# Kernel tuning notes

Measured on AMD Instinct MI355X. Metric: run time of the kernel, lower is better.

## Reference

```python
import jax, jax.numpy as jnp
import numpy as np
from jax import lax

N_CLASS = 21          # VOC: 20 foreground + background
SCORE_THRESH = 0.05   # 'evaluate' preset
NMS_THRESH = 0.3


def loc2bbox(src_bbox, loc):
    # src_bbox, loc: [N, 4] in (y1, x1, y2, x2) / (dy, dx, dh, dw)
    h = src_bbox[:, 2] - src_bbox[:, 0]
    w = src_bbox[:, 3] - src_bbox[:, 1]
    cy = src_bbox[:, 0] + 0.5 * h
    cx = src_bbox[:, 1] + 0.5 * w
    dy, dx, dh, dw = loc[:, 0], loc[:, 1], loc[:, 2], loc[:, 3]
    ncy = dy * h + cy
    ncx = dx * w + cx
    nh = jnp.exp(dh) * h
    nw = jnp.exp(dw) * w
    return jnp.stack([ncy - 0.5 * nh, ncx - 0.5 * nw,
                      ncy + 0.5 * nh, ncx + 0.5 * nw], axis=1)


def pairwise_iou(boxes):
    # boxes: [R, 4] (y1, x1, y2, x2) -> [R, R]
    area = (boxes[:, 2] - boxes[:, 0]) * (boxes[:, 3] - boxes[:, 1])
    ty1 = jnp.maximum(boxes[:, None, 0], boxes[None, :, 0])
    tx1 = jnp.maximum(boxes[:, None, 1], boxes[None, :, 1])
    ty2 = jnp.minimum(boxes[:, None, 2], boxes[None, :, 2])
    tx2 = jnp.minimum(boxes[:, None, 3], boxes[None, :, 3])
    inter = jnp.clip(ty2 - ty1, 0) * jnp.clip(tx2 - tx1, 0)
    union = area[:, None] + area[None, :] - inter
    return inter / jnp.maximum(union, 1e-10)


def nms_keep(boxes, scores):
    # boxes [R,4], scores [R] for one class. Returns bool keep mask [R]
    # (score-thresholded + greedy NMS), fixed shape (mask instead of gather).
    R = boxes.shape[0]
    valid = scores > SCORE_THRESH
    order = jnp.argsort(-scores)
    b = boxes[order]
    v = valid[order]
    suppress = pairwise_iou(b) > NMS_THRESH  # [R, R]
    idx = jnp.arange(R)

    def body(i, keep):
        sup_by_earlier = jnp.any(keep & suppress[:, i] & (idx < i))
        return keep.at[i].set(v[i] & ~sup_by_earlier)

    keep_sorted = lax.fori_loop(0, R, body, jnp.zeros((R,), bool))
    return jnp.zeros((R,), bool).at[order].set(keep_sorted)


def setup_inputs() -> dict:
    key = jax.random.key(0)
    k1, k2, k3, k4 = jax.random.split(key, 4)
    R = 2000
    size_h, size_w = 600, 800
    roi_cls_loc = jax.random.normal(k1, (R, N_CLASS * 4), jnp.float32)
    roi_scores = jax.random.normal(k2, (R, N_CLASS), jnp.float32)
    # valid (y1, x1, y2, x2) rois inside the image
    yx = jax.random.uniform(k3, (R, 2), jnp.float32) * jnp.array([size_h - 32.0, size_w - 32.0])
    hw = 16.0 + jax.random.uniform(k4, (R, 2), jnp.float32) * 128.0
    rois = jnp.concatenate([yx, yx + hw], axis=1)
    return {"roi_cls_loc": roi_cls_loc, "roi_scores": roi_scores,
            "rois": rois, "size_h": size_h, "size_w": size_w}


def reference(roi_cls_loc, roi_scores, rois, size_h, size_w):
    R = rois.shape[0]
    mean = jnp.tile(jnp.asarray([0.0, 0.0, 0.0, 0.0], roi_cls_loc.dtype), N_CLASS)
    std = jnp.tile(jnp.asarray([0.1, 0.1, 0.2, 0.2], roi_cls_loc.dtype), N_CLASS)
    loc = roi_cls_loc * std + mean                      # [R, 4*C]
    loc = loc.reshape(R * N_CLASS, 4)
    src = jnp.broadcast_to(rois[:, None, :], (R, N_CLASS, 4)).reshape(R * N_CLASS, 4)
    box = loc2bbox(src, loc).reshape(R, N_CLASS, 4)
    # clamp y coords (0,2) to [0, H], x coords (1,3) to [0, W]
    y = jnp.clip(box[..., 0::2], 0.0, float(size_h))
    x = jnp.clip(box[..., 1::2], 0.0, float(size_w))
    box = jnp.stack([y[..., 0], x[..., 0], y[..., 1], x[..., 1]], axis=-1)
    prob = jax.nn.softmax(roi_scores, axis=1)           # [R, C]
    # foreground classes only (skip background class 0)
    cls_box = jnp.transpose(box[:, 1:, :], (1, 0, 2))   # [C-1, R, 4]
    cls_prob = prob[:, 1:].T                            # [C-1, R]
    keep = jax.vmap(nms_keep)(lax.stop_gradient(cls_box),
                              lax.stop_gradient(cls_prob))  # [C-1, R] bool
    kept = keep.astype(box.dtype)[..., None]
    # fixed-shape detections: per-class boxes + score, zeroed where suppressed
    out = jnp.concatenate([cls_box * kept, cls_prob[..., None] * kept], axis=-1)
    return out  # [C-1, R, 5]
```

## Files before the change

### kernel.cpp

```cpp
#include <hip/hip_runtime.h>
#include <math.h>

#define NCLS 21
#define NCO 20
#define SUB 8
#define TPB 256
#define STH 1024
#define RCAP 2048
#define RMAX 2000
#define LDSW 7680
#define SCORE_THRESH 0.05f

typedef unsigned long long u64;
typedef unsigned int u32;
typedef unsigned short u16;

#define IOU_MID (20132661.0 / 67108864.0)

__device__ __forceinline__ u64 readlane64(u64 v, int l) {
    u32 lo = (u32)__builtin_amdgcn_readlane((int)(u32)v, l);
    u32 hi = (u32)__builtin_amdgcn_readlane((int)(u32)(v >> 32), l);
    return ((u64)hi << 32) | lo;
}
__device__ __forceinline__ float readlanef(float v, int l) {
    return __uint_as_float((u32)__builtin_amdgcn_readlane((int)__float_as_uint(v), l));
}
__device__ __forceinline__ u64 shflxor64(u64 v, int m) {
    u32 lo = (u32)__shfl_xor((int)(u32)v, m, 64);
    u32 hi = (u32)__shfl_xor((int)(u32)(v >> 32), m, 64);
    return ((u64)hi << 32) | lo;
}

__device__ __forceinline__ int coff(int ic, int nw) {
    return ((ic * nw - ((ic * (ic - 1)) >> 1)) << 6);
}

__device__ __forceinline__ void decode_box(
    const float* __restrict__ rois, const float* __restrict__ loc,
    int r, int cls, float sh, float sw,
    float& by1, float& bx1, float& by2, float& bx2)
{
    float4 rb = *(const float4*)(rois + r * 4);
    float y1 = rb.x, x1 = rb.y, y2 = rb.z, x2 = rb.w;
    float h = y2 - y1, w = x2 - x1;
    float cy = y1 + 0.5f * h, cx = x1 + 0.5f * w;
    float4 l4 = *(const float4*)(loc + r * (NCLS * 4) + cls * 4);
    float dy = l4.x * 0.1f, dx = l4.y * 0.1f;
    float dh = l4.z * 0.2f, dw = l4.w * 0.2f;
    float ncy = dy * h + cy, ncx = dx * w + cx;
    float nh = expf(dh) * h, nw = expf(dw) * w;
    by1 = fminf(fmaxf(ncy - 0.5f * nh, 0.f), sh);
    bx1 = fminf(fmaxf(ncx - 0.5f * nw, 0.f), sw);
    by2 = fminf(fmaxf(ncy + 0.5f * nh, 0.f), sh);
    bx2 = fminf(fmaxf(ncx + 0.5f * nw, 0.f), sw);
}

__device__ __forceinline__ float softmax_p(
    const float* __restrict__ scores, int r, int cls)
{
    const float* srow = scores + r * NCLS;
    float s[NCLS];
    float4 a0 = *(const float4*)(srow);
    float4 a1 = *(const float4*)(srow + 4);
    float4 a2 = *(const float4*)(srow + 8);
    float4 a3 = *(const float4*)(srow + 12);
    float4 a4 = *(const float4*)(srow + 16);
    s[0]=a0.x; s[1]=a0.y; s[2]=a0.z; s[3]=a0.w;
    s[4]=a1.x; s[5]=a1.y; s[6]=a1.z; s[7]=a1.w;
    s[8]=a2.x; s[9]=a2.y; s[10]=a2.z; s[11]=a2.w;
    s[12]=a3.x; s[13]=a3.y; s[14]=a3.z; s[15]=a3.w;
    s[16]=a4.x; s[17]=a4.y; s[18]=a4.z; s[19]=a4.w;
    s[20]=srow[20];
    float m = -INFINITY;
#pragma unroll
    for (int k = 0; k < NCLS; ++k) m = fmaxf(m, s[k]);
    float sum = 0.f, ec = 0.f;
#pragma unroll
    for (int k = 0; k < NCLS; ++k) {
        float e = expf(s[k] - m);
        sum += e;
        if (k == cls) ec = e;
    }
    return ec / sum;
}

__global__ __launch_bounds__(STH) void sort_kernel(
    const float* __restrict__ scores, u64* __restrict__ ord,
    int* __restrict__ nvv, int R)
{
    __shared__ u64 vkey[RCAP];
    __shared__ int cnt;
    const int t = threadIdx.x;
    const int c = blockIdx.x;
    const int lane = t & 63;
    if (t == 0) cnt = 0;
    __syncthreads();

    for (int r = t; r < R; r += STH) {
        float p = softmax_p(scores, r, c + 1);
        bool valid = (p > SCORE_THRESH);
        u64 key = ((u64)(~__float_as_uint(p)) << 32) | (u32)r;
        u64 bal = __ballot(valid);
        if (bal) {
            int nb = (int)__popcll(bal);
            int base = 0;
            if (lane == 0) base = atomicAdd(&cnt, nb);
            base = __shfl(base, 0, 64);
            if (valid)
                vkey[base + (int)__popcll(bal & ((1ull << lane) - 1ull))] = key;
        }
    }
    __syncthreads();
    const int nv = cnt;
    if (t == 0) nvv[c] = nv;

    for (int ibase = 0; ibase < nv; ibase += STH) {
        int i = ibase + t;
        if (i < nv) {
            u64 kj = vkey[i];
            int rank = 0;
#pragma unroll 4
            for (int j = 0; j < nv; ++j)
                rank += (vkey[j] < kj);
            ord[((size_t)c << 11) + rank] = kj;
        }
    }
}

__global__ __launch_bounds__(TPB) void mask_kernel(
    const float* __restrict__ loc, const float* __restrict__ rois,
    const int* __restrict__ ph, const int* __restrict__ pw,
    const u64* __restrict__ ord, const int* __restrict__ nvv,
    u64* __restrict__ M, int R)
{
    __shared__ float4 pb[RCAP];
    __shared__ float ar[RCAP];
    const int t = threadIdx.x;
    const int c = blockIdx.x >> 3;
    const int s = blockIdx.x & 7;
    const int nv = nvv[c];
    const int nw = (nv + 63) >> 6;
    const float sh = (float)(*ph), sw = (float)(*pw);

    for (int i = t; i < nv; i += TPB) {
        u64 key = ord[((size_t)c << 11) + i];
        int r = (int)(u32)key;
        float a0, a1, a2, a3;
        decode_box(rois, loc, r, c + 1, sh, sw, a0, a1, a2, a3);
        pb[i] = make_float4(a0, a1, a2, a3);
        ar[i] = (a2 - a0) * (a3 - a1);
    }
    __syncthreads();

    const int lane = t & 63;
    const int wid = (s << 2) | (t >> 6);
    const int ntasks = nw * (nw + 1) / 2;
    u64* Mc = M + ((size_t)c << 16);
    for (int task = wid; task < ntasks; task += SUB * 4) {
        int ic = 0, rm = task;
        while (rm >= nw - ic) { rm -= nw - ic; ++ic; }
        int v = ic + rm;
        int i = (ic << 6) + lane;
        float4 a = pb[i];
        float iarea = ar[i];
        float4 rj = pb[(v << 6) + lane];
        float ja_l = ar[(v << 6) + lane];
        int jcnt = min(64, nv - (v << 6));
        u64 m = 0;
        for (int jj = 0; jj < jcnt; ++jj) {
            float jy1 = readlanef(rj.x, jj);
            float jx1 = readlanef(rj.y, jj);
            float jy2 = readlanef(rj.z, jj);
            float jx2 = readlanef(rj.w, jj);
            float ja  = readlanef(ja_l, jj);
            float ty1 = fmaxf(a.x, jy1);
            float tx1 = fmaxf(a.y, jx1);
            float ty2 = fminf(a.z, jy2);
            float tx2 = fminf(a.w, jx2);
            float inter = fmaxf(ty2 - ty1, 0.f) * fmaxf(tx2 - tx1, 0.f);
            float uni = fmaxf(iarea + ja - inter, 1e-10f);
            if ((double)inter > IOU_MID * (double)uni) m |= 1ull << jj;
        }
        if (v == ic) m &= (lane < 63) ? (~0ull << (lane + 1)) : 0ull;
        int W = nw - ic;
        if (i < nv) Mc[coff(ic, nw) + lane * W + (v - ic)] = m;
    }
}

__global__ __launch_bounds__(TPB) void resolveout_kernel(
    const float* __restrict__ loc, const float* __restrict__ rois,
    const int* __restrict__ ph, const int* __restrict__ pw,
    const u64* __restrict__ ord, const int* __restrict__ nvv,
    const u64* __restrict__ M, float* __restrict__ out, int R)
{
    __shared__ u64 mlds[LDSW];
    __shared__ u64 keptw[32];
    const int t = threadIdx.x;
    const int c = blockIdx.x >> 3;
    const int s = blockIdx.x & 7;
    const int nv = nvv[c];
    const int nw = (nv + 63) >> 6;
    const u64* Mc = M + ((size_t)c << 16);
    const int S = coff(nw, nw);
    const bool lds_ok = (S <= LDSW);
    if (t < 32) keptw[t] = 0;

    if (lds_ok) {
        for (int base = 0; base < S; base += 2048) {
            u64 v[8];
#pragma unroll
            for (int j = 0; j < 8; ++j) {
                int k = base + (j << 8) + t;
                v[j] = (k < S) ? Mc[k] : 0ull;
            }
#pragma unroll
            for (int j = 0; j < 8; ++j) {
                int k = base + (j << 8) + t;
                if (k < S) mlds[k] = v[j];
            }
        }
    }
    __syncthreads();

    if (t < 64) {
        const int lane = t;
        auto core = [&](const auto* B) {
            u64 remreg = 0;
            for (int w = 0; w < nw; ++w) {
                const int W = nw - w;
                const int cb = coff(w, nw);
                int i = (w << 6) + lane;
                u64 cw = (i < nv) ? B[cb + lane * W] : 0ull;
                int remn = nv - (w << 6);
                u64 vb = (remn >= 64) ? ~0ull : ((1ull << remn) - 1ull);
                u64 cand = vb & ~readlane64(remreg, w);
                u64 X = cand;
                if (X) {
                    for (int it = 0; it < 64; ++it) {
                        u64 contrib = ((X >> lane) & 1ull) ? cw : 0ull;
#pragma unroll
                        for (int d = 1; d < 64; d <<= 1)
                            contrib |= shflxor64(contrib, d);
                        bool keep = ((cand >> lane) & 1ull) &&
                                    !((contrib >> lane) & 1ull);
                        u64 Xn = __ballot(keep);
                        if (Xn == X) break;
                        X = Xn;
                    }
                    if (lane == 0) keptw[w] = X;
                    bool lact = (lane > w) && (lane < nw);
                    u64 km = X, acc = 0;
                    while (km) {
                        int bs[8];
#pragma unroll
                        for (int g = 0; g < 8; ++g) {
                            bs[g] = km ? (__ffsll(km) - 1) : -1;
                            if (km) km &= km - 1;
                        }
                        u64 tmp[8];
#pragma unroll
                        for (int g = 0; g < 8; ++g)
                            tmp[g] = (bs[g] >= 0 && lact)
                                ? B[cb + bs[g] * W + (lane - w)] : 0ull;
#pragma unroll
                        for (int g = 0; g < 8; ++g) acc |= tmp[g];
                    }
                    if (lact) remreg |= acc;
                }
            }
        };
        if (lds_ok) core(mlds); else core(Mc);
    }
    __syncthreads();

    const int chunk = (R + 7) >> 3;
    const int r0 = s * chunk;
    const int r1 = min(R, r0 + chunk);
    float* slice = out + (size_t)c * R * 5;
    for (int k = r0 * 5 + t; k < r1 * 5; k += TPB) slice[k] = 0.f;
    __syncthreads();

    const float sh = (float)(*ph), sw = (float)(*pw);
    for (int i = t; i < nv; i += TPB) {
        if ((keptw[i >> 6] >> (i & 63)) & 1ull) {
            u64 key = ord[((size_t)c << 11) + i];
            int r = (int)(u32)key;
            if (r >= r0 && r < r1) {
                float v0, v1, v2, v3;
                decode_box(rois, loc, r, c + 1, sh, sw, v0, v1, v2, v3);
                float* p = slice + (size_t)r * 5;
                p[0] = v0; p[1] = v1; p[2] = v2; p[3] = v3;
                p[4] = __uint_as_float(~(u32)(key >> 32));
            }
        }
    }
}

#define NTH 1024
__global__ __launch_bounds__(NTH) void fused_kernel(
    const float* __restrict__ loc, const float* __restrict__ scores,
    const float* __restrict__ rois, const int* __restrict__ ph,
    const int* __restrict__ pw, float* __restrict__ out, int R)
{
    __shared__ u64 vkey[RMAX];
    __shared__ float2 p1[RMAX], p2[RMAX];
    __shared__ u64 chunk[64 * 33];
    __shared__ u64 rem[32];
    __shared__ int cnt;

    const int t = threadIdx.x;
    const int lane = t & 63;
    const int c = blockIdx.x + 1;
    const float sh = (float)(*ph), sw = (float)(*pw);

    if (t == 0) cnt = 0;
    if (t < 32) rem[t] = 0;
    __syncthreads();

    for (int r = t; r < R; r += NTH) {
        float p = softmax_p(scores, r, c);
        if (p > SCORE_THRESH) {
            int j = atomicAdd(&cnt, 1);
            vkey[j] = ((u64)(~__float_as_uint(p)) << 32) | (u32)r;
        }
    }
    __syncthreads();
    const int nv = cnt;
    const int nw = (nv + 63) >> 6;

    u64 kk0 = 0, kk1 = 0;
    int r0 = 0, r1 = 0;
    bool in0 = (t < nv), in1 = (t + NTH < nv);
    if (in0) kk0 = vkey[t];
    if (in1) kk1 = vkey[t + NTH];
#pragma unroll 8
    for (int i = 0; i < nv; ++i) {
        u64 k = vkey[i];
        r0 += (k < kk0);
        r1 += (k < kk1);
    }
    __syncthreads();

    for (int u = 0; u < 2; ++u) {
        bool act = u ? in1 : in0;
        if (act) {
            u64 kk = u ? kk1 : kk0;
            int rank = u ? r1 : r0;
            int r = (int)(kk & 0xffffffffu);
            float b0, b1, b2, b3;
            decode_box(rois, loc, r, c, sh, sw, b0, b1, b2, b3);
            vkey[rank] = kk;
            p1[rank] = make_float2(b0, b1);
            p2[rank] = make_float2(b2, b3);
        }
    }
    __syncthreads();

    for (int w = 0; w < nw; ++w) {
        int nwr = nw - w;
        u64 remw = rem[w];
        for (int task = t; task < (nwr << 6); task += NTH) {
            int vr = task >> 6, il = task & 63;
            int i = (w << 6) + il;
            u64 m = 0;
            if (i < nv && !((remw >> il) & 1ull)) {
                int v = w + vr;
                u64 rv = rem[v];
                if (~rv != 0ull) {
                    float2 a1 = p1[i], a2 = p2[i];
                    float iarea = (a2.x - a1.x) * (a2.y - a1.y);
                    int j0 = v << 6;
                    int jhi = min(64, nv - j0);
#pragma unroll 4
                    for (int jj = 0; jj < jhi; ++jj) {
                        float2 b1 = p1[j0 + jj], b2 = p2[j0 + jj];
                        float ty1 = fmaxf(a1.x, b1.x);
                        float tx1 = fmaxf(a1.y, b1.y);
                        float ty2 = fminf(a2.x, b2.x);
                        float tx2 = fminf(a2.y, b2.y);
                        float inter = fmaxf(ty2 - ty1, 0.f) * fmaxf(tx2 - tx1, 0.f);
                        float jarea = (b2.x - b1.x) * (b2.y - b1.y);
                        float uni = fmaxf(iarea + jarea - inter, 1e-10f);
                        if ((double)inter > IOU_MID * (double)uni) m |= 1ull << jj;
                    }
                    if (vr == 0)
                        m &= (il < 63) ? (~0ull << (il + 1)) : 0ull;
                }
            }
            chunk[il * 33 + vr] = m;
        }
        __syncthreads();

        u64 cand = chunk[lane * 33];
        u64 cur = rem[w];
        int remn = nv - (w << 6);
        u64 vb = (remn >= 64) ? ~0ull : ((1ull << remn) - 1ull);
        u64 avail = vb & ~cur;
        u64 kept = 0;
        while (avail) {
            int bb = __ffsll(avail) - 1;
            kept |= 1ull << bb;
            cur |= __shfl(cand, bb, 64);
            avail &= ~(cur | (1ull << bb));
        }
        int vr = t & 31, pg = t >> 5;
        if (vr >= 1 && vr < nwr) {
            u64 acc = 0, km = kept;
            int n = 0;
            while (km) {
                int bb = __ffsll(km) - 1;
                km &= km - 1;
                if ((n & 31) == pg) acc |= chunk[bb * 33 + vr];
                ++n;
            }
            if (acc) atomicOr(&rem[w + vr], acc);
        }
        if (t == 0) rem[w] = cur;
        __syncthreads();
    }

    u16* inv = (u16*)chunk;
    for (int r = t; r < R; r += NTH) inv[r] = 0xffffu;
    __syncthreads();
    for (int i = t; i < nv; i += NTH)
        if (!((rem[i >> 6] >> (i & 63)) & 1ull))
            inv[(int)(vkey[i] & 0xffffffffu)] = (u16)i;
    __syncthreads();
    float* slice = out + (size_t)(c - 1) * R * 5;
    for (int r = t; r < R; r += NTH) {
        int i = inv[r];
        float v0 = 0.f, v1 = 0.f, v2 = 0.f, v3 = 0.f, v4 = 0.f;
        if (i != 0xffff) {
            float2 a1 = p1[i], a2 = p2[i];
            v0 = a1.x; v1 = a1.y; v2 = a2.x; v3 = a2.y;
            v4 = __uint_as_float(~(u32)(vkey[i] >> 32));
        }
        float* p = slice + (size_t)r * 5;
        p[0] = v0; p[1] = v1; p[2] = v2; p[3] = v3; p[4] = v4;
    }
}

extern "C" void kernel_launch(void* const* d_in, const int* in_sizes, int n_in,
                              void* d_out, int out_size, void* d_ws, size_t ws_size,
                              hipStream_t stream) {
    const float* loc    = (const float*)d_in[0];
    const float* scores = (const float*)d_in[1];
    const float* rois   = (const float*)d_in[2];
    const int*   ph     = (const int*)d_in[3];
    const int*   pw     = (const int*)d_in[4];
    float* out = (float*)d_out;
    int R = in_sizes[2] / 4;

    size_t needM   = (size_t)NCO * RCAP * 32 * 8;
    size_t needOrd = (size_t)NCO * RCAP * 8;
    size_t need    = needM + needOrd + 128;

    if (R <= RCAP && ws_size >= need) {
        char* w   = (char*)d_ws;
        u64* M    = (u64*)w;
        u64* ordp = (u64*)(w + needM);
        int* nvv  = (int*)(w + needM + needOrd);
        sort_kernel<<<NCO, STH, 0, stream>>>(scores, ordp, nvv, R);
        mask_kernel<<<NCO * SUB, TPB, 0, stream>>>(loc, rois, ph, pw, ordp, nvv,
                                                   M, R);
        resolveout_kernel<<<NCO * SUB, TPB, 0, stream>>>(loc, rois, ph, pw,
                                                         ordp, nvv, M, out, R);
    } else if (R <= RMAX) {
        fused_kernel<<<NCO, NTH, 0, stream>>>(loc, scores, rois, ph, pw, out, R);
    }
}
```

Baseline: 127.4 us.

## Fuse sort, mask and resolve kernels into one block per class

Merges the three-kernel pipeline (sort, IoU mask build, greedy resolve plus output) into a single 1024-thread kernel with one block per class. LDS is reused for sorted keys, decoded boxes and then the mask matrix. This removes two kernel launches and the inter-kernel global round trips for counts and keys. In exchange the mask stage drops from 160 blocks (32 waves per class) to 20 blocks (16 waves per class), and output zeroing is no longer spread across 8 blocks per class, which costs parallelism.

Measured after the change: 171.1 us. +34.3%, slower.

```diff
diff --git a/kernel.cpp b/kernel.cpp
--- a/kernel.cpp
+++ b/kernel.cpp
@@ -3,8 +3,6 @@
 
 #define NCLS 21
 #define NCO 20
-#define SUB 8
-#define TPB 256
 #define STH 1024
 #define RCAP 2048
 #define RMAX 2000
@@ -84,16 +82,24 @@
     return ec / sum;
 }
 
-__global__ __launch_bounds__(STH) void sort_kernel(
-    const float* __restrict__ scores, u64* __restrict__ ord,
-    int* __restrict__ nvv, int R)
+__global__ __launch_bounds__(STH) void fused_all_kernel(
+    const float* __restrict__ loc, const float* __restrict__ scores,
+    const float* __restrict__ rois, const int* __restrict__ ph,
+    const int* __restrict__ pw, u64* __restrict__ ord,
+    u64* __restrict__ M, float* __restrict__ out, int R)
 {
-    __shared__ u64 vkey[RCAP];
+    __shared__ u64 smem[LDSW];
+    __shared__ u64 keptw[32];
     __shared__ int cnt;
     const int t = threadIdx.x;
     const int c = blockIdx.x;
     const int lane = t & 63;
+    const float sh = (float)(*ph), sw = (float)(*pw);
+    u64* vkey = smem;
+    float4* pb = (float4*)(smem + 2048);
+    float* ar = (float*)(smem + 6144);
     if (t == 0) cnt = 0;
+    if (t < 32) keptw[t] = 0;
     __syncthreads();
 
     for (int r = t; r < R; r += STH) {
@@ -112,39 +118,31 @@
     }
     __syncthreads();
     const int nv = cnt;
-    if (t == 0) nvv[c] = nv;
-
+    const int nw = (nv + 63) >> 6;
+
+    u64 kjs[2]; int rks[2]; int nb2 = 0;
     for (int ibase = 0; ibase < nv; ibase += STH) {
         int i = ibase + t;
+        u64 kj = 0; int rank = -1;
         if (i < nv) {
-            u64 kj = vkey[i];
-            int rank = 0;
+            kj = vkey[i];
+            rank = 0;
 #pragma unroll 4
             for (int j = 0; j < nv; ++j)
                 rank += (vkey[j] < kj);
-            ord[((size_t)c << 11) + rank] = kj;
-        }
-    }
-}
-
-__global__ __launch_bounds__(TPB) void mask_kernel(
-    const float* __restrict__ loc, const float* __restrict__ rois,
-    const int* __restrict__ ph, const int* __restrict__ pw,
-    const u64* __restrict__ ord, const int* __restrict__ nvv,
-    u64* __restrict__ M, int R)
-{
-    __shared__ float4 pb[RCAP];
-    __shared__ float ar[RCAP];
-    const int t = threadIdx.x;
-    const int c = blockIdx.x >> 3;
-    const int s = blockIdx.x & 7;
-    const int nv = nvv[c];
-    const int nw = (nv + 63) >> 6;
-    const float sh = (float)(*ph), sw = (float)(*pw);
-
-    for (int i = t; i < nv; i += TPB) {
-        u64 key = ord[((size_t)c << 11) + i];
-        int r = (int)(u32)key;
+        }
+        kjs[nb2] = kj; rks[nb2] = rank; ++nb2;
+    }
+    __syncthreads();
+    for (int b = 0; b < nb2; ++b)
+        if (rks[b] >= 0) {
+            vkey[rks[b]] = kjs[b];
+            ord[((size_t)c << 11) + rks[b]] = kjs[b];
+        }
+    __syncthreads();
+
+    for (int i = t; i < nv; i += STH) {
+        int r = (int)(u32)vkey[i];
         float a0, a1, a2, a3;
         decode_box(rois, loc, r, c + 1, sh, sw, a0, a1, a2, a3);
         pb[i] = make_float4(a0, a1, a2, a3);
@@ -152,11 +150,10 @@
     }
     __syncthreads();
 
-    const int lane = t & 63;
-    const int wid = (s << 2) | (t >> 6);
+    const int wid = t >> 6;
     const int ntasks = nw * (nw + 1) / 2;
     u64* Mc = M + ((size_t)c << 16);
-    for (int task = wid; task < ntasks; task += SUB * 4) {
+    for (int task = wid; task < ntasks; task += 16) {
         int ic = 0, rm = task;
         while (rm >= nw - ic) { rm -= nw - ic; ++ic; }
         int v = ic + rm;
@@ -185,45 +182,15 @@
         int W = nw - ic;
         if (i < nv) Mc[coff(ic, nw) + lane * W + (v - ic)] = m;
     }
-}
-
-__global__ __launch_bounds__(TPB) void resolveout_kernel(
-    const float* __restrict__ loc, const float* __restrict__ rois,
-    const int* __restrict__ ph, const int* __restrict__ pw,
-    const u64* __restrict__ ord, const int* __restrict__ nvv,
-    const u64* __restrict__ M, float* __restrict__ out, int R)
-{
-    __shared__ u64 mlds[LDSW];
-    __shared__ u64 keptw[32];
-    const int t = threadIdx.x;
-    const int c = blockIdx.x >> 3;
-    const int s = blockIdx.x & 7;
-    const int nv = nvv[c];
-    const int nw = (nv + 63) >> 6;
-    const u64* Mc = M + ((size_t)c << 16);
+    __syncthreads();
+
     const int S = coff(nw, nw);
     const bool lds_ok = (S <= LDSW);
-    if (t < 32) keptw[t] = 0;
-
-    if (lds_ok) {
-        for (int base = 0; base < S; base += 2048) {
-            u64 v[8];
-#pragma unroll
-            for (int j = 0; j < 8; ++j) {
-                int k = base + (j << 8) + t;
-                v[j] = (k < S) ? Mc[k] : 0ull;
-            }
-#pragma unroll
-            for (int j = 0; j < 8; ++j) {
-                int k = base + (j << 8) + t;
-                if (k < S) mlds[k] = v[j];
-            }
-        }
-    }
+    if (lds_ok)
+        for (int k = t; k < S; k += STH) smem[k] = Mc[k];
     __syncthreads();
 
     if (t < 64) {
-        const int lane = t;
         auto core = [&](const auto* B) {
             u64 remreg = 0;
             for (int w = 0; w < nw; ++w) {
@@ -269,29 +236,22 @@
                 }
             }
         };
-        if (lds_ok) core(mlds); else core(Mc);
-    }
-    __syncthreads();
-
-    const int chunk = (R + 7) >> 3;
-    const int r0 = s * chunk;
-    const int r1 = min(R, r0 + chunk);
+        if (lds_ok) core(smem); else core(Mc);
+    }
+    __syncthreads();
+
     float* slice = out + (size_t)c * R * 5;
-    for (int k = r0 * 5 + t; k < r1 * 5; k += TPB) slice[k] = 0.f;
-    __syncthreads();
-
-    const float sh = (float)(*ph), sw = (float)(*pw);
-    for (int i = t; i < nv; i += TPB) {
+    for (int k = t; k < R * 5; k += STH) slice[k] = 0.f;
+    __syncthreads();
+    for (int i = t; i < nv; i += STH) {
         if ((keptw[i >> 6] >> (i & 63)) & 1ull) {
             u64 key = ord[((size_t)c << 11) + i];
             int r = (int)(u32)key;
-            if (r >= r0 && r < r1) {
-                float v0, v1, v2, v3;
-                decode_box(rois, loc, r, c + 1, sh, sw, v0, v1, v2, v3);
-                float* p = slice + (size_t)r * 5;
-                p[0] = v0; p[1] = v1; p[2] = v2; p[3] = v3;
-                p[4] = __uint_as_float(~(u32)(key >> 32));
-            }
+            float v0, v1, v2, v3;
+            decode_box(rois, loc, r, c + 1, sh, sw, v0, v1, v2, v3);
+            float* p = slice + (size_t)r * 5;
+            p[0] = v0; p[1] = v1; p[2] = v2; p[3] = v3;
+            p[4] = __uint_as_float(~(u32)(key >> 32));
         }
     }
 }
@@ -459,12 +419,8 @@
         char* w   = (char*)d_ws;
         u64* M    = (u64*)w;
         u64* ordp = (u64*)(w + needM);
-        int* nvv  = (int*)(w + needM + needOrd);
-        sort_kernel<<<NCO, STH, 0, stream>>>(scores, ordp, nvv, R);
-        mask_kernel<<<NCO * SUB, TPB, 0, stream>>>(loc, rois, ph, pw, ordp, nvv,
-                                                   M, R);
-        resolveout_kernel<<<NCO * SUB, TPB, 0, stream>>>(loc, rois, ph, pw,
-                                                         ordp, nvv, M, out, R);
+        fused_all_kernel<<<NCO, STH, 0, stream>>>(loc, scores, rois, ph, pw,
+                                                  ordp, M, out, R);
     } else if (R <= RMAX) {
         fused_kernel<<<NCO, NTH, 0, stream>>>(loc, scores, rois, ph, pw, out, R);
     }
```
